# Performance work log

Measured on AMD Instinct MI355X. Metric: run time of the kernel, lower is better.

## Reference

```python
import jax, jax.numpy as jnp
import numpy as np

TOP_K = 2  # init top_k


def setup_inputs() -> dict:
    key = jax.random.key(0)
    ks = jax.random.split(key, 6)
    B, S, D, F, E = 4, 4096, 1024, 4096, 8
    return {
        "x": jax.random.normal(ks[0], (B, S, D), dtype=jnp.float32),
        "W_base": jax.random.normal(ks[1], (F, D), dtype=jnp.float32) * 0.02,
        "W_delta": jax.random.normal(ks[2], (F, D), dtype=jnp.float32) * 0.02,
        "bias": jax.random.normal(ks[3], (F,), dtype=jnp.float32) * 0.01,
        "alpha": jax.random.uniform(ks[4], (E,), dtype=jnp.float32),
        "beta": jax.random.uniform(ks[5], (E,), dtype=jnp.float32),
    }


def reference(x, W_base, W_delta, bias, alpha, beta):
    # Reconstructed per-expert encoder weight: W_e = alpha_e*W_base + beta_e*W_delta  [E,F,D]
    W = alpha[:, None, None] * W_base[None] + beta[:, None, None] * W_delta[None]
    mu_w = W.mean(axis=1)                 # column-wise mean   [E,D]
    var_w = W.var(axis=1)                 # biased variance    [E,D]
    bias_mean = bias.mean()
    # Fused batched stats: mu_h, sigma_h for all experts at once  [B,S,E]
    mu_h = jnp.einsum('bsd,ed->bse', x, mu_w) + bias_mean
    sigma_h = jnp.sqrt(jnp.einsum('bsd,ed->bse', x * x, var_w) + 1e-8)
    z = mu_h / (jnp.sqrt(jnp.asarray(2.0, x.dtype)) * sigma_h)
    router_logits = jax.lax.erf(z)        # sparsity scores    [B,S,E]
    # Top-k gating: softmax over top-k logits, scattered back to [B,S,E]
    top_v, top_i = jax.lax.top_k(router_logits, TOP_K)
    soft = jax.nn.softmax(top_v, axis=-1)                       # [B,S,K]
    onehot = jax.nn.one_hot(top_i, router_logits.shape[-1], dtype=soft.dtype)  # [B,S,K,E]
    router_weights = jnp.einsum('bsk,bske->bse', soft, onehot)
    return router_weights, router_logits
```

## Files before the change

kernel.cpp:

```cpp
#include <hip/hip_runtime.h>
#include <math.h>

#define DD 1024
#define FF 4096
#define NTOK 16384


template<int CTRL, int RMASK>
__device__ __forceinline__ float dppadd(float v) {
    int m = __builtin_amdgcn_update_dpp(0, __float_as_int(v), CTRL, RMASK, 0xF, false);
    return v + __int_as_float(m);
}
__device__ __forceinline__ float wave_sum64(float v) {
    v = dppadd<0x121, 0xF>(v);
    v = dppadd<0x122, 0xF>(v);
    v = dppadd<0x124, 0xF>(v);
    v = dppadd<0x128, 0xF>(v);
    v = dppadd<0x142, 0xA>(v);
    v = dppadd<0x143, 0xC>(v);
    return __int_as_float(__builtin_amdgcn_readlane(__float_as_int(v), 63));
}

__device__ __forceinline__ float sel4(int t, float a, float b, float c, float d) {
    float lo = (t & 1) ? b : a;
    float hi = (t & 1) ? d : c;
    return (t & 2) ? hi : lo;
}

__global__ __launch_bounds__(256) void stats1_kernel(
    const float* __restrict__ Wb, const float* __restrict__ Wd,
    const float* __restrict__ bias, float* __restrict__ ws)
{
    const int tx = threadIdx.x;
    const int ty = threadIdx.y;
    const int bx = blockIdx.x;
    const int by = blockIdx.y;
    const int c4 = bx * 64 + tx;

    const float4* Wb4 = (const float4*)Wb;
    const float4* Wd4 = (const float4*)Wd;

    float4 sb  = make_float4(0.f,0.f,0.f,0.f);
    float4 sd  = sb, sbb = sb, sdd = sb, sbd = sb;

    const int row0 = by * 32 + ty * 8;
    #pragma unroll
    for (int r = 0; r < 8; ++r) {
        const int row = row0 + r;
        float4 b = Wb4[row * 256 + c4];
        float4 d = Wd4[row * 256 + c4];
        sb.x += b.x; sb.y += b.y; sb.z += b.z; sb.w += b.w;
        sd.x += d.x; sd.y += d.y; sd.z += d.z; sd.w += d.w;
        sbb.x += b.x*b.x; sbb.y += b.y*b.y; sbb.z += b.z*b.z; sbb.w += b.w*b.w;
        sdd.x += d.x*d.x; sdd.y += d.y*d.y; sdd.z += d.z*d.z; sdd.w += d.w*d.w;
        sbd.x += b.x*d.x; sbd.y += b.y*d.y; sbd.z += b.z*d.z; sbd.w += b.w*d.w;
    }

    __shared__ float4 red[4][5][64];

    red[ty][0][tx] = sb;
    red[ty][1][tx] = sd;
    red[ty][2][tx] = sbb;
    red[ty][3][tx] = sdd;
    red[ty][4][tx] = sbd;
    __syncthreads();

    if (ty == 0) {
        #pragma unroll
        for (int k = 0; k < 5; ++k) {
            float4 acc = red[0][k][tx];
            #pragma unroll
            for (int g = 1; g < 4; ++g) {
                float4 a = red[g][k][tx];
                acc.x += a.x; acc.y += a.y; acc.z += a.z; acc.w += a.w;
            }
            float* dst = ws + k * DD + c4 * 4;
            atomicAdd(dst + 0, acc.x);
            atomicAdd(dst + 1, acc.y);
            atomicAdd(dst + 2, acc.z);
            atomicAdd(dst + 3, acc.w);
        }
    } else if (ty == 1 && bx == 0 && by == 0) {
        float s = 0.f;
        #pragma unroll
        for (int i = 0; i < 64; ++i) s += bias[tx + 64 * i];
        s = wave_sum64(s);
        if (tx == 0) ws[5120] = s;
    }
}

__global__ __launch_bounds__(256, 4) void router_kernel(
    const float* __restrict__ x,
    const float* __restrict__ alpha, const float* __restrict__ beta,
    const float* __restrict__ ws, float* __restrict__ out)
{
    __shared__ float4 smem[1280];
    float4* s_mb4 = smem;
    float4* s_md4 = smem + 256;
    float4* s_vb4 = smem + 512;
    float4* s_vd4 = smem + 768;
    float4* s_cb4 = smem + 1024;
    float* s_mb = (float*)s_mb4;
    float* s_md = (float*)s_md4;
    float* s_vb = (float*)s_vb4;
    float* s_vd = (float*)s_vd4;
    float* s_cb = (float*)s_cb4;

    const int tid  = threadIdx.x;
    const int lane = tid & 63;
    const int wave = tid >> 6;
    const int gw   = blockIdx.x * 4 + wave;
    const int tok0 = gw * 4;

    const float4* xr = (const float4*)(x) + (size_t)tok0 * 256;

    float4 xv[16];
    #pragma unroll
    for (int it = 0; it < 4; ++it) {
        #pragma unroll
        for (int t = 0; t < 4; ++t)
            xv[it * 4 + t] = xr[t * 256 + it * 64 + lane];
    }

    const float invF = 1.0f / (float)FF;
    const float* fin = ws;

    for (int i = tid; i < DD; i += 256) {
        float sb  = fin[i];
        float sd  = fin[DD + i];
        float sbb = fin[2 * DD + i];
        float sdd = fin[3 * DD + i];
        float sbd = fin[4 * DD + i];
        float mb = sb * invF, md = sd * invF;
        s_mb[i] = mb;
        s_md[i] = md;
        s_vb[i] = fmaxf(sbb * invF - mb * mb, 0.f);
        s_vd[i] = fmaxf(sdd * invF - md * md, 0.f);
        s_cb[i] = sbd * invF - mb * md;
    }
    const float bias_mean = fin[5120] * invF;
    __syncthreads();

    float s1[4], s2[4], t1[4], t2[4], t3[4];
    #pragma unroll
    for (int t = 0; t < 4; ++t) { s1[t]=0.f; s2[t]=0.f; t1[t]=0.f; t2[t]=0.f; t3[t]=0.f; }

    #pragma unroll
    for (int it = 0; it < 4; ++it) {
        const int i4 = it * 64 + lane;
        const float4 mb = s_mb4[i4];
        const float4 md = s_md4[i4];
        const float4 vb = s_vb4[i4];
        const float4 vd = s_vd4[i4];
        const float4 cb = s_cb4[i4];
        #pragma unroll
        for (int t = 0; t < 4; ++t) {
            float4 xvv = xv[it * 4 + t];
            float x2x = xvv.x*xvv.x, x2y = xvv.y*xvv.y, x2z = xvv.z*xvv.z, x2w = xvv.w*xvv.w;
            s1[t] += xvv.x*mb.x + xvv.y*mb.y + xvv.z*mb.z + xvv.w*mb.w;
            s2[t] += xvv.x*md.x + xvv.y*md.y + xvv.z*md.z + xvv.w*md.w;
            t1[t] += x2x*vb.x + x2y*vb.y + x2z*vb.z + x2w*vb.w;
            t2[t] += x2x*vd.x + x2y*vd.y + x2z*vd.z + x2w*vd.w;
            t3[t] += x2x*cb.x + x2y*cb.y + x2z*cb.z + x2w*cb.w;
        }
    }

    float A1[4], A2[4], B1[4], B2[4], B3[4];
    #pragma unroll
    for (int t = 0; t < 4; ++t) {
        A1[t] = wave_sum64(s1[t]);
        A2[t] = wave_sum64(s2[t]);
        B1[t] = wave_sum64(t1[t]);
        B2[t] = wave_sum64(t2[t]);
        B3[t] = wave_sum64(t3[t]);
    }

    const int tt = (lane >> 3) & 3;
    const int e  = lane & 7;
    const float a_e = alpha[e];
    const float b_e = beta[e];

    float S1 = sel4(tt, A1[0], A1[1], A1[2], A1[3]);
    float S2 = sel4(tt, A2[0], A2[1], A2[2], A2[3]);
    float T1 = sel4(tt, B1[0], B1[1], B1[2], B1[3]);
    float T2 = sel4(tt, B2[0], B2[1], B2[2], B2[3]);
    float T3 = sel4(tt, B3[0], B3[1], B3[2], B3[3]);

    float mu  = a_e * S1 + b_e * S2 + bias_mean;
    float var = a_e * a_e * T1 + b_e * b_e * T2 + 2.f * a_e * b_e * T3;
    float z   = mu / sqrtf(2.f * (var + 1e-8f));
    float logit = erff(z);

    const int base = lane & 56;
    float l[8];
    #pragma unroll
    for (int q = 0; q < 8; ++q) l[q] = __shfl(logit, base + q);

    float vmax = l[0]; int i0 = 0;
    #pragma unroll
    for (int q = 1; q < 8; ++q) { if (l[q] > vmax) { vmax = l[q]; i0 = q; } }
    float vsec = -1e30f; int i1 = 0;
    #pragma unroll
    for (int q = 0; q < 8; ++q) { if (q != i0 && l[q] > vsec) { vsec = l[q]; i1 = q; } }

    float e1  = __expf(vsec - vmax);
    float inv = 1.f / (1.f + e1);
    float wtop = inv, wsec = e1 * inv;

    if (lane < 32) {
        const int token = tok0 + tt;
        float w = (e == i0) ? wtop : ((e == i1) ? wsec : 0.f);
        out[(size_t)token * 8 + e] = w;
        out[(size_t)NTOK * 8 + (size_t)token * 8 + e] = logit;
    }
}

extern "C" void kernel_launch(void* const* d_in, const int* in_sizes, int n_in,
                              void* d_out, int out_size, void* d_ws, size_t ws_size,
                              hipStream_t stream)
{
    const float* x     = (const float*)d_in[0];
    const float* Wb    = (const float*)d_in[1];
    const float* Wd    = (const float*)d_in[2];
    const float* bias  = (const float*)d_in[3];
    const float* alpha = (const float*)d_in[4];
    const float* beta  = (const float*)d_in[5];
    float* out = (float*)d_out;
    float* ws  = (float*)d_ws;

    hipMemsetAsync(ws, 0, (5 * DD + 1) * sizeof(float), stream);

    dim3 b1(64, 4), g1(4, 128);
    stats1_kernel<<<g1, b1, 0, stream>>>(Wb, Wd, bias, ws);

    router_kernel<<<1024, 256, 0, stream>>>(x, alpha, beta, ws, out);
}
```

Before: 146.6 us.

## Fuse stats and router kernels with ticket-ordered blocks and global flag wait

Merges the weight-statistics kernel and the router kernel into a single launch. The first 512 blocks, ordered by an atomic ticket, compute the column statistics and bump a completion flag. Every block prefetches its x rows before spinning on the flag, so the weight reduction overlaps the x loads and one launch boundary disappears. The trade-off is reliance on a cross-block spin-wait, plus extra atomics for the ticket and flag.

```diff
diff --git a/kernel.cpp b/kernel.cpp
--- a/kernel.cpp
+++ b/kernel.cpp
@@ -4,6 +4,7 @@
 #define DD 1024
 #define FF 4096
 #define NTOK 16384
+#define NSTATS 512
 
 
 template<int CTRL, int RMASK>
@@ -27,74 +28,110 @@
     return (t & 2) ? hi : lo;
 }
 
-__global__ __launch_bounds__(256) void stats1_kernel(
+__global__ __launch_bounds__(256, 4) void fused_kernel(
+    const float* __restrict__ x,
     const float* __restrict__ Wb, const float* __restrict__ Wd,
-    const float* __restrict__ bias, float* __restrict__ ws)
-{
-    const int tx = threadIdx.x;
-    const int ty = threadIdx.y;
-    const int bx = blockIdx.x;
-    const int by = blockIdx.y;
-    const int c4 = bx * 64 + tx;
-
-    const float4* Wb4 = (const float4*)Wb;
-    const float4* Wd4 = (const float4*)Wd;
-
-    float4 sb  = make_float4(0.f,0.f,0.f,0.f);
-    float4 sd  = sb, sbb = sb, sdd = sb, sbd = sb;
-
-    const int row0 = by * 32 + ty * 8;
-    #pragma unroll
-    for (int r = 0; r < 8; ++r) {
-        const int row = row0 + r;
-        float4 b = Wb4[row * 256 + c4];
-        float4 d = Wd4[row * 256 + c4];
-        sb.x += b.x; sb.y += b.y; sb.z += b.z; sb.w += b.w;
-        sd.x += d.x; sd.y += d.y; sd.z += d.z; sd.w += d.w;
-        sbb.x += b.x*b.x; sbb.y += b.y*b.y; sbb.z += b.z*b.z; sbb.w += b.w*b.w;
-        sdd.x += d.x*d.x; sdd.y += d.y*d.y; sdd.z += d.z*d.z; sdd.w += d.w*d.w;
-        sbd.x += b.x*d.x; sbd.y += b.y*d.y; sbd.z += b.z*d.z; sbd.w += b.w*d.w;
-    }
-
-    __shared__ float4 red[4][5][64];
-
-    red[ty][0][tx] = sb;
-    red[ty][1][tx] = sd;
-    red[ty][2][tx] = sbb;
-    red[ty][3][tx] = sdd;
-    red[ty][4][tx] = sbd;
-    __syncthreads();
-
-    if (ty == 0) {
-        #pragma unroll
-        for (int k = 0; k < 5; ++k) {
-            float4 acc = red[0][k][tx];
-            #pragma unroll
-            for (int g = 1; g < 4; ++g) {
-                float4 a = red[g][k][tx];
-                acc.x += a.x; acc.y += a.y; acc.z += a.z; acc.w += a.w;
-            }
-            float* dst = ws + k * DD + c4 * 4;
-            atomicAdd(dst + 0, acc.x);
-            atomicAdd(dst + 1, acc.y);
-            atomicAdd(dst + 2, acc.z);
-            atomicAdd(dst + 3, acc.w);
-        }
-    } else if (ty == 1 && bx == 0 && by == 0) {
-        float s = 0.f;
-        #pragma unroll
-        for (int i = 0; i < 64; ++i) s += bias[tx + 64 * i];
-        s = wave_sum64(s);
-        if (tx == 0) ws[5120] = s;
-    }
-}
-
-__global__ __launch_bounds__(256, 4) void router_kernel(
-    const float* __restrict__ x,
+    const float* __restrict__ bias,
     const float* __restrict__ alpha, const float* __restrict__ beta,
-    const float* __restrict__ ws, float* __restrict__ out)
+    float* __restrict__ ws, float* __restrict__ out)
 {
     __shared__ float4 smem[1280];
+    __shared__ int s_ticket;
+
+    const int tid  = threadIdx.x;
+    const int lane = tid & 63;
+    const int wave = tid >> 6;
+
+    unsigned int* flag_p   = (unsigned int*)(ws + 5121);
+    unsigned int* ticket_p = (unsigned int*)(ws + 5122);
+
+    if (tid == 0) s_ticket = (int)atomicAdd(ticket_p, 1u);
+    __syncthreads();
+    const int ticket = s_ticket;
+
+    if (ticket < NSTATS) {
+        const int cx = ticket & 3;
+        const int cy = ticket >> 2;
+        const int c4 = cx * 64 + lane;
+
+        const float4* Wb4 = (const float4*)Wb;
+        const float4* Wd4 = (const float4*)Wd;
+
+        float4 sb  = make_float4(0.f,0.f,0.f,0.f);
+        float4 sd  = sb, sbb = sb, sdd = sb, sbd = sb;
+
+        const int row0 = cy * 32 + wave * 8;
+        #pragma unroll
+        for (int r = 0; r < 8; ++r) {
+            const int row = row0 + r;
+            float4 b = Wb4[row * 256 + c4];
+            float4 d = Wd4[row * 256 + c4];
+            sb.x += b.x; sb.y += b.y; sb.z += b.z; sb.w += b.w;
+            sd.x += d.x; sd.y += d.y; sd.z += d.z; sd.w += d.w;
+            sbb.x += b.x*b.x; sbb.y += b.y*b.y; sbb.z += b.z*b.z; sbb.w += b.w*b.w;
+            sdd.x += d.x*d.x; sdd.y += d.y*d.y; sdd.z += d.z*d.z; sdd.w += d.w*d.w;
+            sbd.x += b.x*d.x; sbd.y += b.y*d.y; sbd.z += b.z*d.z; sbd.w += b.w*d.w;
+        }
+
+        smem[(wave * 5 + 0) * 64 + lane] = sb;
+        smem[(wave * 5 + 1) * 64 + lane] = sd;
+        smem[(wave * 5 + 2) * 64 + lane] = sbb;
+        smem[(wave * 5 + 3) * 64 + lane] = sdd;
+        smem[(wave * 5 + 4) * 64 + lane] = sbd;
+        __syncthreads();
+
+        if (wave == 0) {
+            const int lr  = (lane + ticket) & 63;
+            const int c4r = cx * 64 + lr;
+            #pragma unroll
+            for (int k = 0; k < 5; ++k) {
+                float4 acc = smem[k * 64 + lr];
+                #pragma unroll
+                for (int g = 1; g < 4; ++g) {
+                    float4 a = smem[(g * 5 + k) * 64 + lr];
+                    acc.x += a.x; acc.y += a.y; acc.z += a.z; acc.w += a.w;
+                }
+                float* dst = ws + k * DD + c4r * 4;
+                atomicAdd(dst + 0, acc.x);
+                atomicAdd(dst + 1, acc.y);
+                atomicAdd(dst + 2, acc.z);
+                atomicAdd(dst + 3, acc.w);
+            }
+        } else if (wave == 1 && ticket == 0) {
+            float s = 0.f;
+            #pragma unroll
+            for (int i = 0; i < 64; ++i) s += bias[lane + 64 * i];
+            s = wave_sum64(s);
+            if (lane == 0)
+                __hip_atomic_store(ws + 5120, s, __ATOMIC_RELAXED,
+                                   __HIP_MEMORY_SCOPE_AGENT);
+        }
+        __syncthreads();
+        if (tid == 0) atomicAdd(flag_p, 1u);
+    }
+
+    const int gw   = blockIdx.x * 4 + wave;
+    const int tok0 = gw * 4;
+    const float4* xr = (const float4*)(x) + (size_t)tok0 * 256;
+
+    float4 xv[16];
+    #pragma unroll
+    for (int it = 0; it < 4; ++it) {
+        #pragma unroll
+        for (int t = 0; t < 4; ++t)
+            xv[it * 4 + t] = xr[t * 256 + it * 64 + lane];
+    }
+    asm volatile("" ::: "memory");
+
+    if (tid == 0) {
+        while (__hip_atomic_load(flag_p, __ATOMIC_RELAXED,
+                                 __HIP_MEMORY_SCOPE_AGENT) < NSTATS)
+            __builtin_amdgcn_s_sleep(2);
+        (void)__hip_atomic_load(flag_p, __ATOMIC_ACQUIRE,
+                                __HIP_MEMORY_SCOPE_AGENT);
+    }
+    __syncthreads();
+
     float4* s_mb4 = smem;
     float4* s_md4 = smem + 256;
     float4* s_vb4 = smem + 512;
@@ -105,22 +142,6 @@
     float* s_vb = (float*)s_vb4;
     float* s_vd = (float*)s_vd4;
     float* s_cb = (float*)s_cb4;
-
-    const int tid  = threadIdx.x;
-    const int lane = tid & 63;
-    const int wave = tid >> 6;
-    const int gw   = blockIdx.x * 4 + wave;
-    const int tok0 = gw * 4;
-
-    const float4* xr = (const float4*)(x) + (size_t)tok0 * 256;
-
-    float4 xv[16];
-    #pragma unroll
-    for (int it = 0; it < 4; ++it) {
-        #pragma unroll
-        for (int t = 0; t < 4; ++t)
-            xv[it * 4 + t] = xr[t * 256 + it * 64 + lane];
-    }
 
     const float invF = 1.0f / (float)FF;
     const float* fin = ws;
@@ -228,10 +249,7 @@
     float* out = (float*)d_out;
     float* ws  = (float*)d_ws;
 
-    hipMemsetAsync(ws, 0, (5 * DD + 1) * sizeof(float), stream);
-
-    dim3 b1(64, 4), g1(4, 128);
-    stats1_kernel<<<g1, b1, 0, stream>>>(Wb, Wd, bias, ws);
-
-    router_kernel<<<1024, 256, 0, stream>>>(x, alpha, beta, ws, out);
-}
+    hipMemsetAsync(ws, 0, 5123 * sizeof(float), stream);
+
+    fused_kernel<<<1024, 256, 0, stream>>>(x, Wb, Wd, bias, alpha, beta, ws, out);
+}
```

After: 193.2 us. +31.8%, slower.

## Replace atomic column reduction with two-pass partials and halve tokens per wave

Applied to the files above, without the earlier changes.

The weight-statistics pass now writes per-row-block partial sums to workspace instead of using global atomics, and a new second kernel reduces the 256 partials and the bias mean. This removes the memset and atomic contention but adds an extra launch and a partial-sum buffer round trip. The router kernel now handles 2 tokens per wave instead of 4, with a software-prefetched x load, and raises occupancy to 8 blocks per SIMD across twice as many blocks. The goal is better latency hiding in the memory-bound x read, at the cost of reloading the shared stats table in twice as many blocks.

```diff
diff --git a/kernel.cpp b/kernel.cpp
--- a/kernel.cpp
+++ b/kernel.cpp
@@ -4,6 +4,8 @@
 #define DD 1024
 #define FF 4096
 #define NTOK 16384
+#define NPART 256
+#define FIN (NPART * 5 * DD)
 
 
 template<int CTRL, int RMASK>
@@ -21,15 +23,9 @@
     return __int_as_float(__builtin_amdgcn_readlane(__float_as_int(v), 63));
 }
 
-__device__ __forceinline__ float sel4(int t, float a, float b, float c, float d) {
-    float lo = (t & 1) ? b : a;
-    float hi = (t & 1) ? d : c;
-    return (t & 2) ? hi : lo;
-}
-
 __global__ __launch_bounds__(256) void stats1_kernel(
     const float* __restrict__ Wb, const float* __restrict__ Wd,
-    const float* __restrict__ bias, float* __restrict__ ws)
+    float* __restrict__ ws)
 {
     const int tx = threadIdx.x;
     const int ty = threadIdx.y;
@@ -43,9 +39,9 @@
     float4 sb  = make_float4(0.f,0.f,0.f,0.f);
     float4 sd  = sb, sbb = sb, sdd = sb, sbd = sb;
 
-    const int row0 = by * 32 + ty * 8;
-    #pragma unroll
-    for (int r = 0; r < 8; ++r) {
+    const int row0 = by * 16 + ty * 4;
+    #pragma unroll
+    for (int r = 0; r < 4; ++r) {
         const int row = row0 + r;
         float4 b = Wb4[row * 256 + c4];
         float4 d = Wd4[row * 256 + c4];
@@ -74,22 +70,59 @@
                 float4 a = red[g][k][tx];
                 acc.x += a.x; acc.y += a.y; acc.z += a.z; acc.w += a.w;
             }
-            float* dst = ws + k * DD + c4 * 4;
-            atomicAdd(dst + 0, acc.x);
-            atomicAdd(dst + 1, acc.y);
-            atomicAdd(dst + 2, acc.z);
-            atomicAdd(dst + 3, acc.w);
-        }
-    } else if (ty == 1 && bx == 0 && by == 0) {
+            ((float4*)(ws + by * (5 * DD) + k * DD))[c4] = acc;
+        }
+    }
+}
+
+__global__ __launch_bounds__(256) void stats2_kernel(
+    const float* __restrict__ bias, float* __restrict__ ws)
+{
+    const int tid   = threadIdx.x;
+    const int col   = tid & 15;
+    const int slice = tid >> 4;
+    const int c4    = blockIdx.x * 16 + col;
+
+    const float4* p4 = (const float4*)ws;
+    float4 acc = make_float4(0.f,0.f,0.f,0.f);
+    #pragma unroll 4
+    for (int p = slice * 16; p < slice * 16 + 16; ++p) {
+        float4 a = p4[(size_t)p * 1280 + c4];
+        acc.x += a.x; acc.y += a.y; acc.z += a.z; acc.w += a.w;
+    }
+
+    __shared__ float4 red[16][17];
+    red[slice][col] = acc;
+    __syncthreads();
+
+    if (slice == 0) {
+        float4 a = red[0][col];
+        #pragma unroll
+        for (int s = 1; s < 16; ++s) {
+            float4 b = red[s][col];
+            a.x += b.x; a.y += b.y; a.z += b.z; a.w += b.w;
+        }
+        ((float4*)(ws + FIN))[c4] = a;
+    }
+
+    if (blockIdx.x == 0) {
         float s = 0.f;
         #pragma unroll
-        for (int i = 0; i < 64; ++i) s += bias[tx + 64 * i];
-        s = wave_sum64(s);
-        if (tx == 0) ws[5120] = s;
-    }
-}
-
-__global__ __launch_bounds__(256, 4) void router_kernel(
+        for (int i = 0; i < 16; ++i) s += bias[tid + 256 * i];
+        #pragma unroll
+        for (int off = 32; off > 0; off >>= 1) s += __shfl_xor(s, off);
+        __shared__ float bws[4];
+        if ((tid & 63) == 0) bws[tid >> 6] = s;
+        __syncthreads();
+        if (tid == 0) ws[FIN + 5120] = bws[0] + bws[1] + bws[2] + bws[3];
+    }
+}
+
+__device__ __forceinline__ float sel2(int t, float a, float b) {
+    return t ? b : a;
+}
+
+__global__ __launch_bounds__(256, 8) void router_kernel(
     const float* __restrict__ x,
     const float* __restrict__ alpha, const float* __restrict__ beta,
     const float* __restrict__ ws, float* __restrict__ out)
@@ -110,20 +143,18 @@
     const int lane = tid & 63;
     const int wave = tid >> 6;
     const int gw   = blockIdx.x * 4 + wave;
-    const int tok0 = gw * 4;
+    const int tok0 = gw * 2;
 
     const float4* xr = (const float4*)(x) + (size_t)tok0 * 256;
 
-    float4 xv[16];
-    #pragma unroll
-    for (int it = 0; it < 4; ++it) {
-        #pragma unroll
-        for (int t = 0; t < 4; ++t)
-            xv[it * 4 + t] = xr[t * 256 + it * 64 + lane];
-    }
+    float4 xp0[2], xp1[2];
+    #pragma unroll
+    for (int t = 0; t < 2; ++t) xp0[t] = xr[t * 256 + 0 * 64 + lane];
+    #pragma unroll
+    for (int t = 0; t < 2; ++t) xp1[t] = xr[t * 256 + 1 * 64 + lane];
 
     const float invF = 1.0f / (float)FF;
-    const float* fin = ws;
+    const float* fin = ws + FIN;
 
     for (int i = tid; i < DD; i += 256) {
         float sb  = fin[i];
@@ -141,9 +172,9 @@
     const float bias_mean = fin[5120] * invF;
     __syncthreads();
 
-    float s1[4], s2[4], t1[4], t2[4], t3[4];
-    #pragma unroll
-    for (int t = 0; t < 4; ++t) { s1[t]=0.f; s2[t]=0.f; t1[t]=0.f; t2[t]=0.f; t3[t]=0.f; }
+    float s1[2], s2[2], t1[2], t2[2], t3[2];
+    #pragma unroll
+    for (int t = 0; t < 2; ++t) { s1[t]=0.f; s2[t]=0.f; t1[t]=0.f; t2[t]=0.f; t3[t]=0.f; }
 
     #pragma unroll
     for (int it = 0; it < 4; ++it) {
@@ -154,20 +185,27 @@
         const float4 vd = s_vd4[i4];
         const float4 cb = s_cb4[i4];
         #pragma unroll
-        for (int t = 0; t < 4; ++t) {
-            float4 xvv = xv[it * 4 + t];
-            float x2x = xvv.x*xvv.x, x2y = xvv.y*xvv.y, x2z = xvv.z*xvv.z, x2w = xvv.w*xvv.w;
-            s1[t] += xvv.x*mb.x + xvv.y*mb.y + xvv.z*mb.z + xvv.w*mb.w;
-            s2[t] += xvv.x*md.x + xvv.y*md.y + xvv.z*md.z + xvv.w*md.w;
+        for (int t = 0; t < 2; ++t) {
+            float4 xv = (it & 1) ? xp1[t] : xp0[t];
+            float x2x = xv.x*xv.x, x2y = xv.y*xv.y, x2z = xv.z*xv.z, x2w = xv.w*xv.w;
+            s1[t] += xv.x*mb.x + xv.y*mb.y + xv.z*mb.z + xv.w*mb.w;
+            s2[t] += xv.x*md.x + xv.y*md.y + xv.z*md.z + xv.w*md.w;
             t1[t] += x2x*vb.x + x2y*vb.y + x2z*vb.z + x2w*vb.w;
             t2[t] += x2x*vd.x + x2y*vd.y + x2z*vd.z + x2w*vd.w;
             t3[t] += x2x*cb.x + x2y*cb.y + x2z*cb.z + x2w*cb.w;
         }
-    }
-
-    float A1[4], A2[4], B1[4], B2[4], B3[4];
-    #pragma unroll
-    for (int t = 0; t < 4; ++t) {
+        if (it < 2) {
+            #pragma unroll
+            for (int t = 0; t < 2; ++t) {
+                float4 nv = xr[t * 256 + (it + 2) * 64 + lane];
+                if (it & 1) xp1[t] = nv; else xp0[t] = nv;
+            }
+        }
+    }
+
+    float A1[2], A2[2], B1[2], B2[2], B3[2];
+    #pragma unroll
+    for (int t = 0; t < 2; ++t) {
         A1[t] = wave_sum64(s1[t]);
         A2[t] = wave_sum64(s2[t]);
         B1[t] = wave_sum64(t1[t]);
@@ -175,16 +213,16 @@
         B3[t] = wave_sum64(t3[t]);
     }
 
-    const int tt = (lane >> 3) & 3;
+    const int tt = (lane >> 3) & 1;
     const int e  = lane & 7;
     const float a_e = alpha[e];
     const float b_e = beta[e];
 
-    float S1 = sel4(tt, A1[0], A1[1], A1[2], A1[3]);
-    float S2 = sel4(tt, A2[0], A2[1], A2[2], A2[3]);
-    float T1 = sel4(tt, B1[0], B1[1], B1[2], B1[3]);
-    float T2 = sel4(tt, B2[0], B2[1], B2[2], B2[3]);
-    float T3 = sel4(tt, B3[0], B3[1], B3[2], B3[3]);
+    float S1 = sel2(tt, A1[0], A1[1]);
+    float S2 = sel2(tt, A2[0], A2[1]);
+    float T1 = sel2(tt, B1[0], B1[1]);
+    float T2 = sel2(tt, B2[0], B2[1]);
+    float T3 = sel2(tt, B3[0], B3[1]);
 
     float mu  = a_e * S1 + b_e * S2 + bias_mean;
     float var = a_e * a_e * T1 + b_e * b_e * T2 + 2.f * a_e * b_e * T3;
@@ -207,7 +245,7 @@
     float inv = 1.f / (1.f + e1);
     float wtop = inv, wsec = e1 * inv;
 
-    if (lane < 32) {
+    if (lane < 16) {
         const int token = tok0 + tt;
         float w = (e == i0) ? wtop : ((e == i1) ? wsec : 0.f);
         out[(size_t)token * 8 + e] = w;
@@ -228,10 +266,10 @@
     float* out = (float*)d_out;
     float* ws  = (float*)d_ws;
 
-    hipMemsetAsync(ws, 0, (5 * DD + 1) * sizeof(float), stream);
-
-    dim3 b1(64, 4), g1(4, 128);
-    stats1_kernel<<<g1, b1, 0, stream>>>(Wb, Wd, bias, ws);
-
-    router_kernel<<<1024, 256, 0, stream>>>(x, alpha, beta, ws, out);
-}
+    dim3 b1(64, 4), g1(4, 256);
+    stats1_kernel<<<g1, b1, 0, stream>>>(Wb, Wd, ws);
+
+    stats2_kernel<<<80, 256, 0, stream>>>(bias, ws);
+
+    router_kernel<<<2048, 256, 0, stream>>>(x, alpha, beta, ws, out);
+}
```

Result: faster. 130.5 us, median of 3 (-11.0%).
